# Performance work log

Hardware: AMD Instinct MI355X
Metric: run time of the kernel (lower is better)

Reference implementation:

```python
import jax, jax.numpy as jnp
import numpy as np

TEMP = 0.07  # temperature used as logits / 0.07 in the original


def setup_inputs() -> dict:
    key = jax.random.key(0)
    k1, k2, k3 = jax.random.split(key, 3)
    B, N, T, L, D = 8, 128, 8, 6, 256
    meta = jax.random.normal(k1, (B, N, T, L, D), dtype=jnp.float32)
    thing = jax.random.randint(k2, (B, N, T), 0, 2, dtype=jnp.int32)
    label = jax.random.randint(k3, (B, N, T), 0, 40, dtype=jnp.int32)
    return {"meta_weight_for_con": meta, "thing_gt_idx": thing, "label_tmp": label}


def _con_loss(meta, thing, label):
    # meta: [B,N,T,L,D]; thing,label: [B,N,T]
    B, N, T, L, D = meta.shape
    P = N * T
    valid = thing.reshape(B, P).astype(bool)            # [B,P] boolean gt mask
    lab = label.reshape(B, P)                           # [B,P]
    # meta_weight_b[mask] -> [K,L,D]; permute(1,0,2) -> per-layer [K,D].
    # We keep all P positions and mask instead of compacting (jit-friendly).
    w = meta.reshape(B, P, L, D).transpose(0, 2, 1, 3)  # [B,L,P,D]
    w = w / jnp.maximum(jnp.linalg.norm(w, axis=-1, keepdims=True), 1e-12)  # F.normalize
    z = jnp.einsum('blpd,blqd->blpq', w, w) / TEMP      # similarity / temp [B,L,P,P]

    same = lab[:, :, None] == lab[:, None, :]           # [B,P,P]
    vpair = valid[:, :, None] & valid[:, None, :]
    eye = jnp.eye(P, dtype=bool)
    pos_mask = same & (~eye) & vpair                    # positives: same label, not self
    neg_mask = (~same) & vpair                          # negatives: different label

    K = valid.sum(axis=1)                               # [B] ins_num_ per batch
    pos_count = pos_mask.sum(axis=-1)                   # [B,P]
    neg_count = neg_mask.sum(axis=-1)                   # [B,P]

    # --- random positive sample per (batch, layer, row), mirroring np.random.choice ---
    u = jax.random.uniform(jax.random.key(42), (B, L, P))
    r = jnp.floor(u * pos_count[:, None, :].astype(u.dtype)).astype(jnp.int32)
    r = jnp.minimum(r, jnp.maximum(pos_count - 1, 0)[:, None, :])
    ranks = jnp.cumsum(pos_mask, axis=-1) - 1           # rank of each positive in index order
    sel = pos_mask[:, None, :, :] & (ranks[:, None, :, :] == r[..., None])  # [B,L,P,P]
    zp = jnp.sum(jnp.where(sel, z, 0.0), axis=-1)       # chosen positive logit [B,L,P]
    diag = jnp.diagonal(z, axis1=-2, axis2=-1)          # self-sim fallback when no positives
    zp = jnp.where((pos_count > 0)[:, None, :], zp, diag)

    # --- last negative (original pads by repeating the last negative to K-1) ---
    iota = jnp.arange(P)
    idx_last = jnp.max(jnp.where(neg_mask, iota[None, None, :], -1), axis=-1)  # [B,P]
    idx = jnp.broadcast_to(jnp.maximum(idx_last, 0)[:, None, :, None], (B, L, P, 1))
    zl = jnp.take_along_axis(z, idx, axis=-1)[..., 0]   # [B,L,P]

    # --- stable CE with label 0: loss = lse(logits) - zp ---
    max_n = jnp.max(jnp.where(neg_mask[:, None], z, -jnp.inf), axis=-1)  # [B,L,P]
    m = jnp.maximum(zp, max_n)
    m = jnp.where(jnp.isfinite(m), m, zp)
    sum_neg = jnp.sum(jnp.where(neg_mask[:, None], jnp.exp(z - m[..., None]), 0.0), axis=-1)
    pad = jnp.maximum((K[:, None] - 1 - neg_count), 0).astype(z.dtype)   # [B,P]
    pad_term = pad[:, None, :] * jnp.where((neg_count > 0)[:, None, :], jnp.exp(zl - m), 0.0)
    loss_row = m + jnp.log(jnp.exp(zp - m) + sum_neg + pad_term) - zp    # [B,L,P]

    row_w = valid.astype(z.dtype)
    mean_per = jnp.sum(loss_row * row_w[:, None, :], axis=-1) / jnp.maximum(K, 1)[:, None].astype(z.dtype)  # [B,L]

    gate = jnp.sum((thing.sum(axis=2) > 0), axis=1) >= 2  # skip batches with <2 gt rows
    return jnp.sum(jnp.where(gate[:, None], mean_per, 0.0))


def reference(meta_weight_for_con, thing_gt_idx, label_tmp):
    return _con_loss(meta_weight_for_con, thing_gt_idx, label_tmp)
```

## Files before the change

### kernel.cpp

```cpp
#include <hip/hip_runtime.h>
#include <stdint.h>

namespace {

constexpr int Bb = 8, Ll = 6, Dd = 256, Pp = 1024;
constexpr float SCALE_Y = 14.285714285714286f * 1.4426950408889634f;
constexpr float M0y = 21.0f;
constexpr float LN2f = 0.6931471805599453f;

typedef __attribute__((ext_vector_type(8))) short short8;
typedef __attribute__((ext_vector_type(4))) float floatx4;

__device__ const int PAIRS[36] = {
  0x00,0x01,0x02,0x03,0x04,0x05,0x06,0x07,
  0x11,0x12,0x13,0x14,0x15,0x16,0x17,
  0x22,0x23,0x24,0x25,0x26,0x27,
  0x33,0x34,0x35,0x36,0x37,
  0x44,0x45,0x46,0x47,
  0x55,0x56,0x57,
  0x66,0x67,
  0x77
};

__device__ __forceinline__ void async16(const void* g, void* l) {
  __builtin_amdgcn_global_load_lds(
      (const __attribute__((address_space(1))) void*)g,
      (__attribute__((address_space(3))) void*)l, 16, 0, 0);
}

__device__ __forceinline__ uint32_t rotl32(uint32_t x, int n) {
  return (x << n) | (x >> (32 - n));
}
__device__ __forceinline__ void tf_round(uint32_t& x0, uint32_t& x1, int r) {
  x0 += x1; x1 = rotl32(x1, r); x1 ^= x0;
}
__device__ void threefry2x32(uint32_t x0, uint32_t x1, uint32_t& o0, uint32_t& o1) {
  const uint32_t k0 = 0u, k1 = 42u;
  const uint32_t k2 = k0 ^ k1 ^ 0x1BD11BDAu;
  x0 += k0; x1 += k1;
  tf_round(x0,x1,13); tf_round(x0,x1,15); tf_round(x0,x1,26); tf_round(x0,x1,6);
  x0 += k1; x1 += k2 + 1u;
  tf_round(x0,x1,17); tf_round(x0,x1,29); tf_round(x0,x1,16); tf_round(x0,x1,24);
  x0 += k2; x1 += k0 + 2u;
  tf_round(x0,x1,13); tf_round(x0,x1,15); tf_round(x0,x1,26); tf_round(x0,x1,6);
  x0 += k0; x1 += k1 + 3u;
  tf_round(x0,x1,17); tf_round(x0,x1,29); tf_round(x0,x1,16); tf_round(x0,x1,24);
  x0 += k1; x1 += k2 + 4u;
  tf_round(x0,x1,13); tf_round(x0,x1,15); tf_round(x0,x1,26); tf_round(x0,x1,6);
  x0 += k2; x1 += k0 + 5u;
  o0 = x0; o1 = x1;
}
__device__ float jax_u01(uint32_t idx) {
  const uint32_t HALF = (uint32_t)(Bb * Ll * Pp / 2);
  uint32_t o0, o1, bits;
  if (idx < HALF) { threefry2x32(idx, idx + HALF, o0, o1); bits = o0; }
  else            { threefry2x32(idx - HALF, idx, o0, o1); bits = o1; }
  return __uint_as_float((bits >> 9) | 0x3f800000u) - 1.0f;
}

__device__ __forceinline__ unsigned short bf16rne(float x) {
  uint32_t u = __float_as_uint(x);
  return (unsigned short)((u + 0x7FFFu + ((u >> 16) & 1u)) >> 16);
}
__device__ __forceinline__ float bf16tof(unsigned short h) {
  return __uint_as_float(((uint32_t)h) << 16);
}

constexpr int NB_NORM = Bb * Pp * Ll / 4;
constexpr int NB_ROW  = Bb * Pp / 4;

__global__ void prep_k(const float* __restrict__ meta, const int* __restrict__ thing,
                       const int* __restrict__ label, unsigned short* __restrict__ wn,
                       int* __restrict__ qpos, int* __restrict__ negc,
                       int* __restrict__ qidx, int* __restrict__ Kv,
                       int* __restrict__ gatev, float* __restrict__ rowsum_g,
                       float* __restrict__ out) {
  __shared__ int sK[256], sG[256];
  const int bid = blockIdx.x, t = threadIdx.x;

  if (bid < NB_NORM) {
    const int wid = (bid * 256 + t) >> 6;
    const int lane = t & 63;
    const float4 v = *(const float4*)(meta + (size_t)wid * Dd + lane * 4);
    float ss = v.x * v.x + v.y * v.y + v.z * v.z + v.w * v.w;
    #pragma unroll
    for (int m = 32; m; m >>= 1) ss += __shfl_xor(ss, m, 64);
    const float inv = 1.0f / fmaxf(sqrtf(ss), 1e-12f);
    const int bp = wid / Ll, l = wid - bp * Ll;
    const int b = bp >> 10, p = bp & (Pp - 1);
    unsigned short* dst = wn + ((size_t)(b * Ll + l) * Pp + p) * Dd + lane * 4;
    ushort4 o;
    o.x = bf16rne(v.x * inv); o.y = bf16rne(v.y * inv);
    o.z = bf16rne(v.z * inv); o.w = bf16rne(v.w * inv);
    *(ushort4*)dst = o;
    return;
  }
  if (bid < NB_NORM + NB_ROW) {
    const int wid = (bid - NB_NORM) * 4 + (t >> 6);
    const int lane = t & 63;
    const int b = wid >> 10, p = wid & (Pp - 1);
    const int* lab = label + b * Pp;
    const int* th  = thing + b * Pp;
    const int myLab = lab[p];
    const bool myValid = (th[p] != 0);

    uint32_t posbits = 0;
    int cnt[16];
    int pc = 0, nc = 0, last = -1;
    #pragma unroll
    for (int c = 0; c < 16; ++c) {
      const int q = c * 64 + lane;
      const int lq = lab[q];
      const bool vq = (th[q] != 0);
      const bool same = (lq == myLab);
      const bool pos = myValid && vq && same && (q != p);
      const bool neg = myValid && vq && !same;
      uint64_t bp2 = __ballot(pos);
      uint64_t bn = __ballot(neg);
      if (pos) posbits |= (1u << c);
      cnt[c] = __popcll(bp2);
      pc += cnt[c];
      nc += __popcll(bn);
      if (bn) last = c * 64 + 63 - __clzll(bn);
    }
    int qsel[Ll];
    #pragma unroll
    for (int l = 0; l < Ll; ++l) qsel[l] = p;
    if (pc > 0) {
      for (int l = 0; l < Ll; ++l) {
        const float u = jax_u01((uint32_t)((b * Ll + l) * Pp + p));
        int r = (int)floorf(u * (float)pc);
        r = min(r, pc - 1);
        int base = 0;
        for (int c = 0; c < 16; ++c) {
          if (r < base + cnt[c]) {
            const bool mine = (posbits >> c) & 1u;
            uint64_t bm = __ballot(mine);
            uint64_t ltmask = (lane == 0) ? 0ull : (~0ull >> (64 - lane));
            int myrank = __popcll(bm & ltmask);
            bool hit = mine && (base + myrank == r);
            uint64_t hb = __ballot(hit);
            qsel[l] = c * 64 + (int)__builtin_ctzll(hb);
            break;
          }
          base += cnt[c];
        }
      }
    }
    if (lane == 0) {
      negc[wid] = nc;
      qidx[wid] = (last < 0) ? 0 : last;
      #pragma unroll
      for (int l = 0; l < Ll; ++l) qpos[(b * Ll + l) * Pp + p] = qsel[l];
    }
    return;
  }
  if (bid < NB_NORM + NB_ROW + Bb) {
    const int b = bid - (NB_NORM + NB_ROW);
    int k = 0;
    for (int p = t; p < Pp; p += 256) k += (thing[b * Pp + p] != 0);
    int g = 0;
    if (t < 128) {
      int any = 0;
      for (int tt = 0; tt < 8; ++tt) any |= (thing[(b * 128 + t) * 8 + tt] != 0);
      g = any;
    }
    sK[t] = k; sG[t] = g;
    __syncthreads();
    for (int s = 128; s; s >>= 1) {
      if (t < s) { sK[t] += sK[t + s]; sG[t] += sG[t + s]; }
      __syncthreads();
    }
    if (t == 0) { Kv[b] = sK[0]; gatev[b] = (sG[0] >= 2) ? 1 : 0; }
    return;
  }
  if (bid < NB_NORM + NB_ROW + Bb + 48) {
    const int idx = (bid - (NB_NORM + NB_ROW + Bb)) * 256 + t;
    *(float4*)(rowsum_g + idx * 4) = (float4){0.f, 0.f, 0.f, 0.f};
    return;
  }
  if (t == 0) out[0] = 0.f;
}

__global__ void zpzl_k(const unsigned short* __restrict__ wn,
                       const int* __restrict__ qpos, const int* __restrict__ qidx,
                       float* __restrict__ zp_g, float* __restrict__ zl_g) {
  const int wid = blockIdx.x * 4 + (threadIdx.x >> 6);
  const int lane = threadIdx.x & 63;
  const int bl = wid >> 10, p = wid & (Pp - 1);
  const int b = bl / Ll;
  const int qp = qpos[bl * Pp + p];
  const int qi = qidx[b * Pp + p];
  const unsigned short* W = wn + (size_t)bl * Pp * Dd;
  const ushort4 a  = *(const ushort4*)(W + (size_t)p  * Dd + lane * 4);
  const ushort4 vb = *(const ushort4*)(W + (size_t)qp * Dd + lane * 4);
  const ushort4 vc = *(const ushort4*)(W + (size_t)qi * Dd + lane * 4);
  const float ax = bf16tof(a.x), ay = bf16tof(a.y), az = bf16tof(a.z), aw = bf16tof(a.w);
  float sp = ax * bf16tof(vb.x) + ay * bf16tof(vb.y) + az * bf16tof(vb.z) + aw * bf16tof(vb.w);
  float sl = ax * bf16tof(vc.x) + ay * bf16tof(vc.y) + az * bf16tof(vc.z) + aw * bf16tof(vc.w);
  #pragma unroll
  for (int m = 32; m; m >>= 1) {
    sp += __shfl_xor(sp, m, 64);
    sl += __shfl_xor(sl, m, 64);
  }
  if (lane == 0) {
    zp_g[bl * Pp + p] = sp * SCALE_Y;
    zl_g[bl * Pp + p] = sl * SCALE_Y;
  }
}

__global__ __launch_bounds__(256)
void gemm_loss_k(const unsigned short* __restrict__ wn,
                 const int* __restrict__ thing, const int* __restrict__ label,
                 float* __restrict__ rowsum_g) {
  __shared__ __align__(16) unsigned short As[128 * 64];
  __shared__ __align__(16) unsigned short Bs[128 * 64];
  __shared__ int labp_s[128], valp_s[128], labq_s[128], valq_s[128];
  __shared__ float rowsum_lds[128], colsum_lds[128];

  const int t = threadIdx.x;
  const int bl = blockIdx.y;
  const int b = bl / Ll;
  const int pair = PAIRS[blockIdx.x];
  const int pt = pair >> 4, qt = pair & 15;
  const bool diag = (pt == qt);
  const int p0 = pt * 128, q0 = qt * 128;

  if (t < 128) {
    labp_s[t] = label[b * Pp + p0 + t];
    valp_s[t] = thing[b * Pp + p0 + t];
    labq_s[t] = label[b * Pp + q0 + t];
    valq_s[t] = thing[b * Pp + q0 + t];
    rowsum_lds[t] = 0.f;
    colsum_lds[t] = 0.f;
  }

  const unsigned short* Wbl = wn + (size_t)bl * Pp * Dd;
  const int lane = t & 63;
  const int w = t >> 6, wr = w >> 1, wc = w & 1;
  const int cq = lane & 15, rq = lane >> 4;
  const int wbase16 = (t & ~63) * 16;

  floatx4 acc[4][4];
  #pragma unroll
  for (int i = 0; i < 4; ++i)
    #pragma unroll
    for (int j = 0; j < 4; ++j) acc[i][j] = (floatx4){0.f, 0.f, 0.f, 0.f};

  const char* Bbase = diag ? (const char*)As : (const char*)Bs;

  for (int k0 = 0; k0 < Dd; k0 += 64) {
    __syncthreads();
    #pragma unroll
    for (int it = 0; it < 4; ++it) {
      const int c = it * 256 + t;
      const int row = c >> 3, sp = c & 7;
      const int sl = sp ^ (row & 7);
      async16(Wbl + (size_t)(p0 + row) * Dd + k0 + sl * 8, (char*)As + it * 4096 + wbase16);
      if (!diag)
        async16(Wbl + (size_t)(q0 + row) * Dd + k0 + sl * 8, (char*)Bs + it * 4096 + wbase16);
    }
    __syncthreads();
    #pragma unroll
    for (int sub = 0; sub < 2; ++sub) {
      short8 af[4], bf[4];
      #pragma unroll
      for (int fi = 0; fi < 4; ++fi) {
        const int row = wr * 64 + fi * 16 + cq;
        const int sp = (sub * 4 + rq) ^ (row & 7);
        af[fi] = *(const short8*)((const char*)As + row * 128 + sp * 16);
      }
      #pragma unroll
      for (int fj = 0; fj < 4; ++fj) {
        const int row = wc * 64 + fj * 16 + cq;
        const int sp = (sub * 4 + rq) ^ (row & 7);
        bf[fj] = *(const short8*)(Bbase + row * 128 + sp * 16);
      }
      #pragma unroll
      for (int fi = 0; fi < 4; ++fi)
        #pragma unroll
        for (int fj = 0; fj < 4; ++fj)
          acc[fi][fj] = __builtin_amdgcn_mfma_f32_16x16x32_bf16(af[fi], bf[fj],
                                                                acc[fi][fj], 0, 0, 0);
    }
  }

  int qlabv[4];
  float qvalf[4];
  float csum[4] = {0.f, 0.f, 0.f, 0.f};
  #pragma unroll
  for (int fj = 0; fj < 4; ++fj) {
    const int cl = wc * 64 + fj * 16 + cq;
    qlabv[fj] = labq_s[cl];
    qvalf[fj] = valq_s[cl] ? 1.f : 0.f;
  }
  #pragma unroll
  for (int fi = 0; fi < 4; ++fi) {
    #pragma unroll
    for (int reg = 0; reg < 4; ++reg) {
      const int rl = wr * 64 + fi * 16 + rq * 4 + reg;
      const int rlab = labp_s[rl];
      const float rvalf = valp_s[rl] ? 1.f : 0.f;
      float rsum = 0.f;
      #pragma unroll
      for (int fj = 0; fj < 4; ++fj) {
        const float y = acc[fi][fj][reg] * SCALE_Y;
        const float negm = (qlabv[fj] != rlab) ? (qvalf[fj] * rvalf) : 0.f;
        const float term = negm * exp2f(y - M0y);
        rsum += term;
        csum[fj] += term;
      }
      rsum += __shfl_xor(rsum, 1); rsum += __shfl_xor(rsum, 2);
      rsum += __shfl_xor(rsum, 4); rsum += __shfl_xor(rsum, 8);
      if (cq == 0) atomicAdd(&rowsum_lds[rl], rsum);
    }
  }
  if (!diag) {
    #pragma unroll
    for (int fj = 0; fj < 4; ++fj) {
      float c = csum[fj];
      c += __shfl_xor(c, 16); c += __shfl_xor(c, 32);
      if (rq == 0) atomicAdd(&colsum_lds[wc * 64 + fj * 16 + cq], c);
    }
  }
  __syncthreads();
  if (t < 128) {
    atomicAdd(&rowsum_g[bl * Pp + p0 + t], rowsum_lds[t]);
    if (!diag) atomicAdd(&rowsum_g[bl * Pp + q0 + t], colsum_lds[t]);
  }
}

__global__ void finalize_k(const float* __restrict__ rowsum_g, const float* __restrict__ zp_g,
                           const float* __restrict__ zl_g, const int* __restrict__ negc,
                           const int* __restrict__ thing, const int* __restrict__ Kv,
                           const int* __restrict__ gatev, float* __restrict__ out) {
  const int bl = blockIdx.x, b = bl / Ll, t = threadIdx.x;
  const int Kb = Kv[b];
  const float invK = 1.f / (float)max(Kb, 1);
  float acc = 0.f;
  for (int p = t; p < Pp; p += 256) {
    if (thing[b * Pp + p] != 0) {
      const float yp = zp_g[bl * Pp + p], yl = zl_g[bl * Pp + p];
      const float rs = rowsum_g[bl * Pp + p];
      const int nc = negc[b * Pp + p];
      const float pad = fmaxf((float)(Kb - 1 - nc), 0.f);
      const float tot = exp2f(yp - M0y) + rs + ((nc > 0) ? pad * exp2f(yl - M0y) : 0.f);
      acc += LN2f * (M0y + log2f(tot) - yp) * invK;
    }
  }
  __shared__ float sb[256];
  sb[t] = acc;
  __syncthreads();
  for (int s = 128; s; s >>= 1) {
    if (t < s) sb[t] += sb[t + s];
    __syncthreads();
  }
  if (t == 0 && gatev[b]) atomicAdd(out, sb[0]);
}

}

extern "C" void kernel_launch(void* const* d_in, const int* in_sizes, int n_in,
                              void* d_out, int out_size, void* d_ws, size_t ws_size,
                              hipStream_t stream) {
  const float* meta = (const float*)d_in[0];
  const int* thing  = (const int*)d_in[1];
  const int* label  = (const int*)d_in[2];
  float* out = (float*)d_out;

  char* ws = (char*)d_ws;
  size_t off = 0;
  unsigned short* wn = (unsigned short*)(ws + off); off += (size_t)Bb * Ll * Pp * Dd * 2;
  int* qpos  = (int*)(ws + off); off += (size_t)Bb * Ll * Pp * 4;
  int* negc  = (int*)(ws + off); off += (size_t)Bb * Pp * 4;
  int* qidx  = (int*)(ws + off); off += (size_t)Bb * Pp * 4;
  int* Kv    = (int*)(ws + off); off += 64;
  int* gatev = (int*)(ws + off); off += 64;
  float* rowsum_g = (float*)(ws + off); off += (size_t)Bb * Ll * Pp * 4;
  float* zp_g     = (float*)(ws + off); off += (size_t)Bb * Ll * Pp * 4;
  float* zl_g     = (float*)(ws + off); off += (size_t)Bb * Ll * Pp * 4;

  const int nb_prep = NB_NORM + NB_ROW + Bb + 48 + 1;
  prep_k<<<nb_prep, 256, 0, stream>>>(meta, thing, label, wn, qpos, negc, qidx,
                                      Kv, gatev, rowsum_g, out);
  zpzl_k<<<(Bb * Ll * Pp) / 4, 256, 0, stream>>>(wn, qpos, qidx, zp_g, zl_g);
  {
    dim3 grid(36, Bb * Ll);
    gemm_loss_k<<<grid, 256, 0, stream>>>(wn, thing, label, rowsum_g);
  }
  finalize_k<<<Bb * Ll, 256, 0, stream>>>(rowsum_g, zp_g, zl_g, negc, thing, Kv, gatev, out);
}
```

Measured before the change: 163.0 us.

## Load MFMA fragments directly from global memory instead of staging through LDS

The GEMM tile loop no longer stages A/B tiles into shared memory with async global-to-LDS copies and barriers. Each wave now reads its bf16 MFMA fragments straight from global memory over the full 256-wide K dimension, fully unrolled. This removes LDS traffic, swizzling and per-k-step barriers, and frees LDS for higher occupancy. In exchange, fragments shared between waves are re-fetched redundantly through the cache, and each 16-byte per-lane load is strided by a row.

```diff
diff --git a/kernel.cpp b/kernel.cpp
--- a/kernel.cpp
+++ b/kernel.cpp
@@ -21,12 +21,6 @@
   0x66,0x67,
   0x77
 };
-
-__device__ __forceinline__ void async16(const void* g, void* l) {
-  __builtin_amdgcn_global_load_lds(
-      (const __attribute__((address_space(1))) void*)g,
-      (__attribute__((address_space(3))) void*)l, 16, 0, 0);
-}
 
 __device__ __forceinline__ uint32_t rotl32(uint32_t x, int n) {
   return (x << n) | (x >> (32 - n));
@@ -213,8 +207,6 @@
 void gemm_loss_k(const unsigned short* __restrict__ wn,
                  const int* __restrict__ thing, const int* __restrict__ label,
                  float* __restrict__ rowsum_g) {
-  __shared__ __align__(16) unsigned short As[128 * 64];
-  __shared__ __align__(16) unsigned short Bs[128 * 64];
   __shared__ int labp_s[128], valp_s[128], labq_s[128], valq_s[128];
   __shared__ float rowsum_lds[128], colsum_lds[128];
 
@@ -234,12 +226,20 @@
     rowsum_lds[t] = 0.f;
     colsum_lds[t] = 0.f;
   }
+  __syncthreads();
 
   const unsigned short* Wbl = wn + (size_t)bl * Pp * Dd;
   const int lane = t & 63;
   const int w = t >> 6, wr = w >> 1, wc = w & 1;
   const int cq = lane & 15, rq = lane >> 4;
-  const int wbase16 = (t & ~63) * 16;
+
+  const unsigned short* Ap[4];
+  const unsigned short* Bp[4];
+  #pragma unroll
+  for (int f = 0; f < 4; ++f) {
+    Ap[f] = Wbl + (size_t)(p0 + wr * 64 + f * 16 + cq) * Dd + rq * 8;
+    Bp[f] = Wbl + (size_t)(q0 + wc * 64 + f * 16 + cq) * Dd + rq * 8;
+  }
 
   floatx4 acc[4][4];
   #pragma unroll
@@ -247,42 +247,19 @@
     #pragma unroll
     for (int j = 0; j < 4; ++j) acc[i][j] = (floatx4){0.f, 0.f, 0.f, 0.f};
 
-  const char* Bbase = diag ? (const char*)As : (const char*)Bs;
-
-  for (int k0 = 0; k0 < Dd; k0 += 64) {
-    __syncthreads();
-    #pragma unroll
-    for (int it = 0; it < 4; ++it) {
-      const int c = it * 256 + t;
-      const int row = c >> 3, sp = c & 7;
-      const int sl = sp ^ (row & 7);
-      async16(Wbl + (size_t)(p0 + row) * Dd + k0 + sl * 8, (char*)As + it * 4096 + wbase16);
-      if (!diag)
-        async16(Wbl + (size_t)(q0 + row) * Dd + k0 + sl * 8, (char*)Bs + it * 4096 + wbase16);
-    }
-    __syncthreads();
-    #pragma unroll
-    for (int sub = 0; sub < 2; ++sub) {
-      short8 af[4], bf[4];
+  #pragma unroll
+  for (int sub = 0; sub < 8; ++sub) {
+    short8 af[4], bf[4];
+    #pragma unroll
+    for (int fi = 0; fi < 4; ++fi) af[fi] = *(const short8*)(Ap[fi] + sub * 32);
+    #pragma unroll
+    for (int fj = 0; fj < 4; ++fj) bf[fj] = *(const short8*)(Bp[fj] + sub * 32);
+    #pragma unroll
+    for (int fi = 0; fi < 4; ++fi)
       #pragma unroll
-      for (int fi = 0; fi < 4; ++fi) {
-        const int row = wr * 64 + fi * 16 + cq;
-        const int sp = (sub * 4 + rq) ^ (row & 7);
-        af[fi] = *(const short8*)((const char*)As + row * 128 + sp * 16);
-      }
-      #pragma unroll
-      for (int fj = 0; fj < 4; ++fj) {
-        const int row = wc * 64 + fj * 16 + cq;
-        const int sp = (sub * 4 + rq) ^ (row & 7);
-        bf[fj] = *(const short8*)(Bbase + row * 128 + sp * 16);
-      }
-      #pragma unroll
-      for (int fi = 0; fi < 4; ++fi)
-        #pragma unroll
-        for (int fj = 0; fj < 4; ++fj)
-          acc[fi][fj] = __builtin_amdgcn_mfma_f32_16x16x32_bf16(af[fi], bf[fj],
-                                                                acc[fi][fj], 0, 0, 0);
-    }
+      for (int fj = 0; fj < 4; ++fj)
+        acc[fi][fj] = __builtin_amdgcn_mfma_f32_16x16x32_bf16(af[fi], bf[fj],
+                                                              acc[fi][fj], 0, 0, 0);
   }
 
   int qlabv[4];
```

Measured after the change: 181.8 us. 1.12x slower.
